# Optimization experiments

Hardware: AMD Instinct MI355X
Metric: run time of the kernel (lower is better)

## Reference

```python
import jax, jax.numpy as jnp
import numpy as np

B, N, D_IN, L, H, NB = 4, 512, 32, 64, 128, 2

def setup_inputs() -> dict:
    key = jax.random.key(0)
    ks = jax.random.split(key, 8)
    s = lambda k, shape, fan: jax.random.normal(k, shape, dtype=jnp.float32) / np.float32(np.sqrt(fan))
    return {
        "X": jax.random.normal(ks[0], (B, N, D_IN), dtype=jnp.float32),
        "proj_w": s(ks[1], (D_IN, L), D_IN),
        "proj_b": jnp.zeros((L,), jnp.float32),
        "rn_w1": s(ks[2], (NB, 2 * L, H), 2 * L),
        "rn_b1": jnp.zeros((NB, H), jnp.float32),
        "rn_w2": s(ks[3], (NB, H, L), H),
        "rn_b2": jnp.zeros((NB, L), jnp.float32),
        "fc_w1": s(ks[4], (NB, L, H), L),
        "fc_b1": jnp.zeros((NB, H), jnp.float32),
        "fc_w2": s(ks[5], (NB, H, L), H),
        "fc_b2": jnp.zeros((NB, L), jnp.float32),
        "dec_w": s(ks[6], (L, 1), L),
        "dec_b": jnp.zeros((1,), jnp.float32),
    }

def _rn_block(Z, rw1, rb1, rw2, rb2, fw1, fb1, fw2, fb2):
    # RelationNetwork: pairs[b,n,m] = concat(Y[b,m], X[b,n]) with X=Y=Z.
    # First linear on concat splits into two small GEMMs (Y-half of rw1 first).
    Ldim = Z.shape[-1]
    M = Z.shape[1]
    y_lin = Z @ rw1[:Ldim]          # [B,M,H]  (Y occupies first L cols of pairs)
    x_lin = Z @ rw1[Ldim:]          # [B,N,H]
    h = jax.nn.relu(x_lin[:, :, None, :] + y_lin[:, None, :, :] + rb1)  # [B,N,M,H]
    # sum-pool over M commutes with the second linear layer
    rn_out = h.sum(axis=2) @ rw2 + M * rb2  # [B,N,L]
    Z = Z + rn_out
    Z = Z + (jax.nn.relu(Z @ fw1 + fb1) @ fw2 + fb2)
    return Z

def reference(X, proj_w, proj_b, rn_w1, rn_b1, rn_w2, rn_b2, fc_w1, fc_b1, fc_w2, fc_b2, dec_w, dec_b):
    Z = X @ proj_w + proj_b  # [B,N,L]
    for i in range(rn_w1.shape[0]):  # fixed small num_blocks
        Z = _rn_block(Z, rn_w1[i], rn_b1[i], rn_w2[i], rn_b2[i],
                      fc_w1[i], fc_b1[i], fc_w2[i], fc_b2[i])
    pooled = Z.sum(axis=1)           # pool2='sum' over set dim
    out = pooled @ dec_w + dec_b     # [B,1]
    return out.squeeze(-1)           # [B]
```

## Files before the change

kernel.cpp:

```cpp
#include <hip/hip_runtime.h>
#include <math.h>

#define B 4
#define N 512
#define DIN 32
#define L 64
#define H 128
#define NB 2
#define R (B * N)

__global__ void k_pair0(const float* __restrict__ X, const float* __restrict__ PW,
                        const float* __restrict__ PB, const float* __restrict__ w1,
                        const float* __restrict__ rb1, float* __restrict__ hsum,
                        float* __restrict__ out) {
    __shared__ float ys[1024];
    __shared__ float ss[N + 1];
    __shared__ float csum[64];
    __shared__ float csuf[65];
    __shared__ float vu[66];

    int t = threadIdx.x;
    int b = blockIdx.x >> 7;
    int h = blockIdx.x & 127;

    if (blockIdx.x == 0 && t < B) out[t] = 0.f;

    if (t < 64) {
        int d = t & 31;
        const float* wcol = w1 + (t < 32 ? 0 : L * H) + h;
        float s = 0.f;
#pragma unroll
        for (int k = 0; k < L; ++k) s += PW[d * L + k] * wcol[(size_t)k * H];
        vu[t] = s;
    } else if (t < 66) {
        const float* wcol = w1 + (t == 64 ? 0 : L * H) + h;
        float s = (t == 64) ? rb1[h] : 0.f;
#pragma unroll
        for (int k = 0; k < L; ++k) s += PB[k] * wcol[(size_t)k * H];
        vu[t] = s;
    }
    __syncthreads();

    float xq0, xq1;
    {
        const float* xr = X + ((size_t)b * N + t) * DIN;
        float ya = vu[64], xa = vu[65];
#pragma unroll
        for (int d = 0; d < DIN; ++d) {
            float xv = xr[d];
            ya += xv * vu[d];
            xa += xv * vu[32 + d];
        }
        ys[t] = ya; xq0 = xa;
        const float* xr2 = X + ((size_t)b * N + t + 256) * DIN;
        float yb = vu[64], xb = vu[65];
#pragma unroll
        for (int d = 0; d < DIN; ++d) {
            float xv = xr2[d];
            yb += xv * vu[d];
            xb += xv * vu[32 + d];
        }
        ys[t + 256] = yb; xq1 = xb;
    }
    for (int m = N + t; m < 1024; m += 256) ys[m] = INFINITY;
    __syncthreads();

    for (int k = 2; k <= N; k <<= 1) {
        for (int j = k >> 1; j > 0; j >>= 1) {
            int i = ((t & ~(j - 1)) << 1) | (t & (j - 1));
            int p = i | j;
            float a = ys[i], c = ys[p];
            bool up = (i & k) == 0;
            if ((a > c) == up) { ys[i] = c; ys[p] = a; }
            __syncthreads();
        }
    }

    if (t < 64) {
        float s = 0.f;
        int base = t * 8;
#pragma unroll
        for (int q = 7; q >= 0; --q) s += ys[base + q];
        csum[t] = s;
    }
    __syncthreads();
    if (t == 0) {
        csuf[64] = 0.f;
        float run = 0.f;
        for (int c = 63; c >= 0; --c) { run += csum[c]; csuf[c] = run; }
    }
    __syncthreads();
    for (int i = t; i < N; i += 256) {
        float s = csuf[(i >> 3) + 1];
        int e = i | 7;
        for (int q = e; q >= i; --q) s += ys[q];
        ss[i] = s;
    }
    if (t == 0) ss[N] = 0.f;
    __syncthreads();

    float* ocol = hsum + (size_t)b * N * H + h;
    float v0 = -xq0, v1 = -xq1;
    int p0 = 0, p1 = 0;
#pragma unroll
    for (int s = 512; s >= 1; s >>= 1) {
        if (ys[p0 + s - 1] <= v0) p0 += s;
        if (ys[p1 + s - 1] <= v1) p1 += s;
    }
    ocol[(size_t)t * H] = (float)(N - p0) * xq0 + ss[p0];
    ocol[(size_t)(t + 256) * H] = (float)(N - p1) * xq1 + ss[p1];
}

__global__ void k_pair1(const float* __restrict__ xlin, const float* __restrict__ ylin,
                        float* __restrict__ hsum) {
    __shared__ float ys[1024];
    __shared__ float ss[N + 1];
    __shared__ float csum[64];
    __shared__ float csuf[65];

    int t = threadIdx.x;
    int b = blockIdx.x >> 7;
    int h = blockIdx.x & 127;

    const float* ycol = ylin + (size_t)b * N * H + h;
    for (int m = t; m < N; m += 256) ys[m] = ycol[(size_t)m * H];
    for (int m = N + t; m < 1024; m += 256) ys[m] = INFINITY;
    __syncthreads();

    for (int k = 2; k <= N; k <<= 1) {
        for (int j = k >> 1; j > 0; j >>= 1) {
            int i = ((t & ~(j - 1)) << 1) | (t & (j - 1));
            int p = i | j;
            float a = ys[i], c = ys[p];
            bool up = (i & k) == 0;
            if ((a > c) == up) { ys[i] = c; ys[p] = a; }
            __syncthreads();
        }
    }

    if (t < 64) {
        float s = 0.f;
        int base = t * 8;
#pragma unroll
        for (int q = 7; q >= 0; --q) s += ys[base + q];
        csum[t] = s;
    }
    __syncthreads();
    if (t == 0) {
        csuf[64] = 0.f;
        float run = 0.f;
        for (int c = 63; c >= 0; --c) { run += csum[c]; csuf[c] = run; }
    }
    __syncthreads();
    for (int i = t; i < N; i += 256) {
        float s = csuf[(i >> 3) + 1];
        int e = i | 7;
        for (int q = e; q >= i; --q) s += ys[q];
        ss[i] = s;
    }
    if (t == 0) ss[N] = 0.f;
    __syncthreads();

    const float* xcol = xlin + (size_t)b * N * H + h;
    float* ocol = hsum + (size_t)b * N * H + h;
    int n0 = t, n1 = t + 256;
    float x0 = xcol[(size_t)n0 * H];
    float x1 = xcol[(size_t)n1 * H];
    float v0 = -x0, v1 = -x1;
    int p0 = 0, p1 = 0;
#pragma unroll
    for (int s = 512; s >= 1; s >>= 1) {
        if (ys[p0 + s - 1] <= v0) p0 += s;
        if (ys[p1 + s - 1] <= v1) p1 += s;
    }
    ocol[(size_t)n0 * H] = (float)(N - p0) * x0 + ss[p0];
    ocol[(size_t)n1 * H] = (float)(N - p1) * x1 + ss[p1];
}

template <bool FINAL, bool FROMX>
__global__ void k_post(const float* __restrict__ hsum, const float* __restrict__ w2,
                       const float* __restrict__ b2, const float* __restrict__ fw1,
                       const float* __restrict__ fb1, const float* __restrict__ fw2,
                       const float* __restrict__ fb2, const float* __restrict__ nw1,
                       const float* __restrict__ nb1, float* __restrict__ Z,
                       float* __restrict__ ylin, float* __restrict__ xlin,
                       const float* __restrict__ X, const float* __restrict__ PW,
                       const float* __restrict__ PB,
                       const float* __restrict__ dw, const float* __restrict__ db,
                       float* __restrict__ out) {
    __shared__ float wbuf[H * L];
    __shared__ float hl_[8 * H];
    __shared__ float zl[8 * L];
    __shared__ float tl[8 * H];
    __shared__ float part[4];

    int t = threadIdx.x;
    int row0 = blockIdx.x * 8;

    ((float4*)hl_)[t] = ((const float4*)(hsum + (size_t)row0 * H))[t];
    if (FROMX) {
        ((float4*)wbuf)[t] = ((const float4*)PW)[t];
        ((float4*)wbuf)[t + 256] = ((const float4*)PW)[t + 256];
        if (t < 64) ((float4*)tl)[t] = ((const float4*)(X + (size_t)row0 * DIN))[t];
        __syncthreads();
        {
            int l = t & 63;
            int r0 = (t >> 6) * 2, r1 = r0 + 1;
            float a0 = PB[l], a1 = a0;
#pragma unroll
            for (int d = 0; d < DIN; ++d) {
                float w = wbuf[d * L + l];
                a0 += tl[r0 * DIN + d] * w;
                a1 += tl[r1 * DIN + d] * w;
            }
            zl[r0 * L + l] = a0;
            zl[r1 * L + l] = a1;
        }
        __syncthreads();
    } else {
        if (t < 128) ((float4*)zl)[t] = ((const float4*)(Z + (size_t)row0 * L))[t];
    }
#pragma unroll
    for (int j = 0; j < 8; ++j)
        ((float4*)wbuf)[t + j * 256] = ((const float4*)w2)[t + j * 256];
    __syncthreads();

    {
        int l = t & 63;
        int r0 = (t >> 6) * 2, r1 = r0 + 1;
        float a0 = 0.f, a1 = 0.f;
#pragma unroll
        for (int kk = 0; kk < H; kk += 4) {
            float4 h0v = *(float4*)&hl_[r0 * H + kk];
            float4 h1v = *(float4*)&hl_[r1 * H + kk];
            float w0 = wbuf[(kk + 0) * L + l];
            float w1v = wbuf[(kk + 1) * L + l];
            float w2v = wbuf[(kk + 2) * L + l];
            float w3 = wbuf[(kk + 3) * L + l];
            a0 += h0v.x * w0 + h0v.y * w1v + h0v.z * w2v + h0v.w * w3;
            a1 += h1v.x * w0 + h1v.y * w1v + h1v.z * w2v + h1v.w * w3;
        }
        float nb2 = (float)N * b2[l];
        zl[r0 * L + l] += a0 + nb2;
        zl[r1 * L + l] += a1 + nb2;
    }
    __syncthreads();
#pragma unroll
    for (int j = 0; j < 8; ++j)
        ((float4*)wbuf)[t + j * 256] = ((const float4*)fw1)[t + j * 256];
    __syncthreads();

    {
        int h = t & 127;
        int rq = (t >> 7) * 4;
        float acc0 = 0.f, acc1 = 0.f, acc2 = 0.f, acc3 = 0.f;
#pragma unroll
        for (int ll = 0; ll < L; ll += 4) {
            float w0 = wbuf[(ll + 0) * H + h];
            float w1v = wbuf[(ll + 1) * H + h];
            float w2v = wbuf[(ll + 2) * H + h];
            float w3 = wbuf[(ll + 3) * H + h];
            float4 z0 = *(float4*)&zl[(rq + 0) * L + ll];
            float4 z1 = *(float4*)&zl[(rq + 1) * L + ll];
            float4 z2 = *(float4*)&zl[(rq + 2) * L + ll];
            float4 z3 = *(float4*)&zl[(rq + 3) * L + ll];
            acc0 += z0.x * w0 + z0.y * w1v + z0.z * w2v + z0.w * w3;
            acc1 += z1.x * w0 + z1.y * w1v + z1.z * w2v + z1.w * w3;
            acc2 += z2.x * w0 + z2.y * w1v + z2.z * w2v + z2.w * w3;
            acc3 += z3.x * w0 + z3.y * w1v + z3.z * w2v + z3.w * w3;
        }
        float bb = fb1[h];
        tl[(rq + 0) * H + h] = fmaxf(acc0 + bb, 0.f);
        tl[(rq + 1) * H + h] = fmaxf(acc1 + bb, 0.f);
        tl[(rq + 2) * H + h] = fmaxf(acc2 + bb, 0.f);
        tl[(rq + 3) * H + h] = fmaxf(acc3 + bb, 0.f);
    }
    __syncthreads();
#pragma unroll
    for (int j = 0; j < 8; ++j)
        ((float4*)wbuf)[t + j * 256] = ((const float4*)fw2)[t + j * 256];
    __syncthreads();

    float zfin0, zfin1;
    int l_ = t & 63;
    int r0_ = (t >> 6) * 2, r1_ = r0_ + 1;
    {
        float a0 = 0.f, a1 = 0.f;
#pragma unroll
        for (int kk = 0; kk < H; kk += 4) {
            float4 t0v = *(float4*)&tl[r0_ * H + kk];
            float4 t1v = *(float4*)&tl[r1_ * H + kk];
            float w0 = wbuf[(kk + 0) * L + l_];
            float w1v = wbuf[(kk + 1) * L + l_];
            float w2v = wbuf[(kk + 2) * L + l_];
            float w3 = wbuf[(kk + 3) * L + l_];
            a0 += t0v.x * w0 + t0v.y * w1v + t0v.z * w2v + t0v.w * w3;
            a1 += t1v.x * w0 + t1v.y * w1v + t1v.z * w2v + t1v.w * w3;
        }
        float bb = fb2[l_];
        zfin0 = zl[r0_ * L + l_] + a0 + bb;
        zfin1 = zl[r1_ * L + l_] + a1 + bb;
    }

    if (FINAL) {
        float v = (zfin0 + zfin1) * dw[l_];
#pragma unroll
        for (int off = 32; off > 0; off >>= 1) v += __shfl_down(v, off);
        if (l_ == 0) part[t >> 6] = v;
        __syncthreads();
        if (t == 0) {
            float s = part[0] + part[1] + part[2] + part[3];
            if ((row0 % N) == 0) s += db[0];
            atomicAdd(out + row0 / N, s);
        }
        return;
    }

    __syncthreads();
    zl[r0_ * L + l_] = zfin0;
    zl[r1_ * L + l_] = zfin1;
    Z[(size_t)(row0 + r0_) * L + l_] = zfin0;
    Z[(size_t)(row0 + r1_) * L + l_] = zfin1;
    __syncthreads();

#pragma unroll
    for (int j = 0; j < 8; ++j)
        ((float4*)wbuf)[t + j * 256] = ((const float4*)nw1)[t + j * 256];
    __syncthreads();
    {
        int h = t & 127;
        int rq = (t >> 7) * 4;
        float acc0 = nb1[h], acc1 = acc0, acc2 = acc0, acc3 = acc0;
#pragma unroll
        for (int kk = 0; kk < L; kk += 4) {
            float w0 = wbuf[(kk + 0) * H + h];
            float w1v = wbuf[(kk + 1) * H + h];
            float w2v = wbuf[(kk + 2) * H + h];
            float w3 = wbuf[(kk + 3) * H + h];
            float4 z0 = *(float4*)&zl[(rq + 0) * L + kk];
            float4 z1 = *(float4*)&zl[(rq + 1) * L + kk];
            float4 z2 = *(float4*)&zl[(rq + 2) * L + kk];
            float4 z3 = *(float4*)&zl[(rq + 3) * L + kk];
            acc0 += z0.x * w0 + z0.y * w1v + z0.z * w2v + z0.w * w3;
            acc1 += z1.x * w0 + z1.y * w1v + z1.z * w2v + z1.w * w3;
            acc2 += z2.x * w0 + z2.y * w1v + z2.z * w2v + z2.w * w3;
            acc3 += z3.x * w0 + z3.y * w1v + z3.z * w2v + z3.w * w3;
        }
        ylin[(size_t)(row0 + rq + 0) * H + h] = acc0;
        ylin[(size_t)(row0 + rq + 1) * H + h] = acc1;
        ylin[(size_t)(row0 + rq + 2) * H + h] = acc2;
        ylin[(size_t)(row0 + rq + 3) * H + h] = acc3;
    }
    __syncthreads();
#pragma unroll
    for (int j = 0; j < 8; ++j)
        ((float4*)wbuf)[t + j * 256] = ((const float4*)(nw1 + L * H))[t + j * 256];
    __syncthreads();
    {
        int h = t & 127;
        int rq = (t >> 7) * 4;
        float acc0 = 0.f, acc1 = 0.f, acc2 = 0.f, acc3 = 0.f;
#pragma unroll
        for (int kk = 0; kk < L; kk += 4) {
            float w0 = wbuf[(kk + 0) * H + h];
            float w1v = wbuf[(kk + 1) * H + h];
            float w2v = wbuf[(kk + 2) * H + h];
            float w3 = wbuf[(kk + 3) * H + h];
            float4 z0 = *(float4*)&zl[(rq + 0) * L + kk];
            float4 z1 = *(float4*)&zl[(rq + 1) * L + kk];
            float4 z2 = *(float4*)&zl[(rq + 2) * L + kk];
            float4 z3 = *(float4*)&zl[(rq + 3) * L + kk];
            acc0 += z0.x * w0 + z0.y * w1v + z0.z * w2v + z0.w * w3;
            acc1 += z1.x * w0 + z1.y * w1v + z1.z * w2v + z1.w * w3;
            acc2 += z2.x * w0 + z2.y * w1v + z2.z * w2v + z2.w * w3;
            acc3 += z3.x * w0 + z3.y * w1v + z3.z * w2v + z3.w * w3;
        }
        xlin[(size_t)(row0 + rq + 0) * H + h] = acc0;
        xlin[(size_t)(row0 + rq + 1) * H + h] = acc1;
        xlin[(size_t)(row0 + rq + 2) * H + h] = acc2;
        xlin[(size_t)(row0 + rq + 3) * H + h] = acc3;
    }
}

extern "C" void kernel_launch(void* const* d_in, const int* in_sizes, int n_in,
                              void* d_out, int out_size, void* d_ws, size_t ws_size,
                              hipStream_t stream) {
    const float* X      = (const float*)d_in[0];
    const float* proj_w = (const float*)d_in[1];
    const float* proj_b = (const float*)d_in[2];
    const float* rn_w1  = (const float*)d_in[3];
    const float* rn_b1  = (const float*)d_in[4];
    const float* rn_w2  = (const float*)d_in[5];
    const float* rn_b2  = (const float*)d_in[6];
    const float* fc_w1  = (const float*)d_in[7];
    const float* fc_b1  = (const float*)d_in[8];
    const float* fc_w2  = (const float*)d_in[9];
    const float* fc_b2  = (const float*)d_in[10];
    const float* dec_w  = (const float*)d_in[11];
    const float* dec_b  = (const float*)d_in[12];
    float* out = (float*)d_out;

    float* ws   = (float*)d_ws;
    float* Z    = ws;
    float* ylin = Z + R * L;
    float* xlin = ylin + R * H;
    float* hsum = xlin + R * H;

    k_pair0<<<B * H, 256, 0, stream>>>(X, proj_w, proj_b, rn_w1, rn_b1, hsum, out);
    k_post<false, true><<<R / 8, 256, 0, stream>>>(
        hsum, rn_w2, rn_b2, fc_w1, fc_b1, fc_w2, fc_b2,
        rn_w1 + 2 * L * H, rn_b1 + H, Z, ylin, xlin,
        X, proj_w, proj_b, nullptr, nullptr, nullptr);
    k_pair1<<<B * H, 256, 0, stream>>>(xlin, ylin, hsum);
    k_post<true, false><<<R / 8, 256, 0, stream>>>(
        hsum, rn_w2 + H * L, rn_b2 + L, fc_w1 + L * H, fc_b1 + H,
        fc_w2 + H * L, fc_b2 + L, nullptr, nullptr, Z, nullptr, nullptr,
        nullptr, nullptr, nullptr, dec_w, dec_b, out);
}
```

Measured before the change: 61.82 us.

## Keep bitonic sort in registers with wavefront shuffles for small strides

Replaces the shared-memory bitonic sort of 512 values with a register-resident version. Each thread holds two elements. Strides under 64 use __shfl_xor within a wavefront, the 256 stride compares the two registers a thread already holds, and only strides 64 and 128 go through shared memory. This removes most of the per-step __syncthreads barriers and LDS traffic, at the cost of two barriers per shared-memory step and a final store back to shared memory.

Result: slower. 70.46 us (+14.0%).

```diff
diff --git a/kernel.cpp b/kernel.cpp
--- a/kernel.cpp
+++ b/kernel.cpp
@@ -8,6 +8,38 @@
 #define H 128
 #define NB 2
 #define R (B * N)
+
+__device__ __forceinline__ void bitonic512_regs(float& va, float& vb,
+                                                float* __restrict__ ys, int t) {
+    const int i1 = t + 256;
+    for (int k = 2; k <= 512; k <<= 1) {
+        for (int j = k >> 1; j >= 1; j >>= 1) {
+            if (j == 256) {
+                float lo = fminf(va, vb), hi = fmaxf(va, vb);
+                va = lo; vb = hi;
+            } else if (j >= 64) {
+                ys[t] = va; ys[i1] = vb;
+                __syncthreads();
+                float pa = ys[t ^ j];
+                float pb = ys[i1 ^ j];
+                __syncthreads();
+                bool ma = ((t & k) == 0) == ((t & j) == 0);
+                bool mb = ((i1 & k) == 0) == ((i1 & j) == 0);
+                va = ma ? fminf(va, pa) : fmaxf(va, pa);
+                vb = mb ? fminf(vb, pb) : fmaxf(vb, pb);
+            } else {
+                float pa = __shfl_xor(va, j);
+                float pb = __shfl_xor(vb, j);
+                bool ma = ((t & k) == 0) == ((t & j) == 0);
+                bool mb = ((i1 & k) == 0) == ((i1 & j) == 0);
+                va = ma ? fminf(va, pa) : fmaxf(va, pa);
+                vb = mb ? fminf(vb, pb) : fmaxf(vb, pb);
+            }
+        }
+    }
+    ys[t] = va; ys[i1] = vb;
+    __syncthreads();
+}
 
 __global__ void k_pair0(const float* __restrict__ X, const float* __restrict__ PW,
                         const float* __restrict__ PB, const float* __restrict__ w1,
@@ -39,9 +71,10 @@
         for (int k = 0; k < L; ++k) s += PB[k] * wcol[(size_t)k * H];
         vu[t] = s;
     }
-    __syncthreads();
-
-    float xq0, xq1;
+    for (int m = N + t; m < 1024; m += 256) ys[m] = INFINITY;
+    __syncthreads();
+
+    float va, vb, xq0, xq1;
     {
         const float* xr = X + ((size_t)b * N + t) * DIN;
         float ya = vu[64], xa = vu[65];
@@ -51,7 +84,7 @@
             ya += xv * vu[d];
             xa += xv * vu[32 + d];
         }
-        ys[t] = ya; xq0 = xa;
+        va = ya; xq0 = xa;
         const float* xr2 = X + ((size_t)b * N + t + 256) * DIN;
         float yb = vu[64], xb = vu[65];
 #pragma unroll
@@ -60,21 +93,10 @@
             yb += xv * vu[d];
             xb += xv * vu[32 + d];
         }
-        ys[t + 256] = yb; xq1 = xb;
-    }
-    for (int m = N + t; m < 1024; m += 256) ys[m] = INFINITY;
-    __syncthreads();
-
-    for (int k = 2; k <= N; k <<= 1) {
-        for (int j = k >> 1; j > 0; j >>= 1) {
-            int i = ((t & ~(j - 1)) << 1) | (t & (j - 1));
-            int p = i | j;
-            float a = ys[i], c = ys[p];
-            bool up = (i & k) == 0;
-            if ((a > c) == up) { ys[i] = c; ys[p] = a; }
-            __syncthreads();
-        }
-    }
+        vb = yb; xq1 = xb;
+    }
+
+    bitonic512_regs(va, vb, ys, t);
 
     if (t < 64) {
         float s = 0.f;
@@ -123,20 +145,11 @@
     int h = blockIdx.x & 127;
 
     const float* ycol = ylin + (size_t)b * N * H + h;
-    for (int m = t; m < N; m += 256) ys[m] = ycol[(size_t)m * H];
+    float va = ycol[(size_t)t * H];
+    float vb = ycol[(size_t)(t + 256) * H];
     for (int m = N + t; m < 1024; m += 256) ys[m] = INFINITY;
-    __syncthreads();
-
-    for (int k = 2; k <= N; k <<= 1) {
-        for (int j = k >> 1; j > 0; j >>= 1) {
-            int i = ((t & ~(j - 1)) << 1) | (t & (j - 1));
-            int p = i | j;
-            float a = ys[i], c = ys[p];
-            bool up = (i & k) == 0;
-            if ((a > c) == up) { ys[i] = c; ys[p] = a; }
-            __syncthreads();
-        }
-    }
+
+    bitonic512_regs(va, vb, ys, t);
 
     if (t < 64) {
         float s = 0.f;
```
